# Kernel tuning notes

Measured on AMD Instinct MI355X. Metric: run time of the kernel, lower is better.

## Reference

```python
import jax, jax.numpy as jnp
import numpy as np

B, N, H, W_SP, DIM, FPN = 16, 4, 32, 32, 1024, 512
EPS = 1e-5

def setup_inputs() -> dict:
    key = jax.random.key(0)
    k1, k2 = jax.random.split(key)
    x = jax.random.normal(k1, (B, N, H, W_SP, DIM), dtype=jnp.float32)
    gamma = jnp.ones((DIM,), dtype=jnp.float32)
    beta = jnp.zeros((DIM,), dtype=jnp.float32)
    W = jax.random.normal(k2, (4 * FPN, DIM), dtype=jnp.float32) * (1.0 / np.sqrt(DIM))
    b = jnp.zeros((4 * FPN,), dtype=jnp.float32)
    return {"x": x, "gamma": gamma, "beta": beta, "W": W, "b": b}

def reference(x, gamma, beta, W, b):
    # LayerNorm over channel dim
    mu = jnp.mean(x, axis=-1, keepdims=True)
    var = jnp.mean(jnp.square(x - mu), axis=-1, keepdims=True)
    xn = (x - mu) * jax.lax.rsqrt(var + EPS) * gamma + beta
    # Linear: dim -> 4*fpn_dim (QLinear with quant=False == nn.Linear)
    y = jnp.einsum('bnhwc,oc->bnhwo', xn, W) + b
    # QAct with quant=False is identity.
    # Patch split: (B,N,H,W,2,2,F) -> (B,N,H,2,W,2,F) -> (B,N,2H,2W,F)
    Bv, Nv, Hv, Wv = y.shape[:4]
    y = y.reshape(Bv, Nv, Hv, Wv, 2, 2, FPN)
    y = jnp.transpose(y, (0, 1, 2, 4, 3, 5, 6))
    return y.reshape(Bv, Nv, 2 * Hv, 2 * Wv, FPN)
```

## Files before the change

kernel.cpp:

```cpp
#include <hip/hip_runtime.h>
#include <hip/hip_bf16.h>
#include <cstdint>
#include <cstddef>

#define M_ROWS 65536
#define K_DIM  1024
#define N_OUT  2048

typedef __attribute__((ext_vector_type(8))) short short8;
typedef __attribute__((ext_vector_type(4))) float floatx4;

__device__ __forceinline__ unsigned short f2bf(float f) {
  unsigned int u = __float_as_uint(f);
  u += 0x7fffu + ((u >> 16) & 1u);
  return (unsigned short)(u >> 16);
}

__global__ __launch_bounds__(256) void ln_bf16_kernel(
    const float* __restrict__ x, const float* __restrict__ gamma,
    const float* __restrict__ beta, ushort* __restrict__ xn) {
  const int wave = threadIdx.x >> 6;
  const int lane = threadIdx.x & 63;
  const size_t row = (size_t)blockIdx.x * 4 + wave;
  const float4* xr = (const float4*)(x + row * K_DIM);
  float4 v[4];
  float s = 0.f, ss = 0.f;
#pragma unroll
  for (int i = 0; i < 4; ++i) {
    v[i] = xr[lane + 64 * i];
    s  += v[i].x + v[i].y + v[i].z + v[i].w;
    ss += v[i].x * v[i].x + v[i].y * v[i].y + v[i].z * v[i].z + v[i].w * v[i].w;
  }
#pragma unroll
  for (int off = 32; off; off >>= 1) {
    s  += __shfl_xor(s, off, 64);
    ss += __shfl_xor(ss, off, 64);
  }
  const float mu = s * (1.0f / 1024.0f);
  const float rstd = rsqrtf(ss * (1.0f / 1024.0f) - mu * mu + 1e-5f);
  ushort4* orow = (ushort4*)(xn + row * K_DIM);
#pragma unroll
  for (int i = 0; i < 4; ++i) {
    const float4 g  = ((const float4*)gamma)[lane + 64 * i];
    const float4 bb = ((const float4*)beta)[lane + 64 * i];
    ushort4 o;
    o.x = f2bf((v[i].x - mu) * rstd * g.x + bb.x);
    o.y = f2bf((v[i].y - mu) * rstd * g.y + bb.y);
    o.z = f2bf((v[i].z - mu) * rstd * g.z + bb.z);
    o.w = f2bf((v[i].w - mu) * rstd * g.w + bb.w);
    orow[lane + 64 * i] = o;
  }
}

__global__ __launch_bounds__(256) void wconv_kernel(const float* __restrict__ W,
                                                    ushort* __restrict__ Wb) {
  const int i = blockIdx.x * 256 + threadIdx.x;
  const float4 w = ((const float4*)W)[i];
  ushort4 o;
  o.x = f2bf(w.x); o.y = f2bf(w.y); o.z = f2bf(w.z); o.w = f2bf(w.w);
  ((ushort4*)Wb)[i] = o;
}

__device__ __forceinline__ void async_copy16(const ushort* g, ushort* l) {
  __builtin_amdgcn_global_load_lds(
      (const __attribute__((address_space(1))) void*)g,
      (__attribute__((address_space(3))) void*)l, 16, 0, 0);
}

__global__ __launch_bounds__(256) void gemm_kernel(
    const ushort* __restrict__ A,
    const ushort* __restrict__ Bw,
    const float* __restrict__ bias, float* __restrict__ out) {
  __shared__ ushort As[128 * 32];
  __shared__ ushort Bs[128 * 32];

  const int tid  = threadIdx.x;
  const int bn   = blockIdx.x;
  const int bm   = blockIdx.y;
  const int lane = tid & 63;
  const int warp = tid >> 6;
  const int quad = lane >> 4;
  const int l16  = lane & 15;
  const int wm   = warp & 1;
  const int wn   = warp >> 1;

  const ushort* aG0 = A  + (size_t)(bm * 128      + (tid >> 2)) * K_DIM + (tid & 3) * 8;
  const ushort* aG1 = A  + (size_t)(bm * 128 + 64 + (tid >> 2)) * K_DIM + (tid & 3) * 8;
  const ushort* bG0 = Bw + (size_t)(bn * 128      + (tid >> 2)) * K_DIM + (tid & 3) * 8;
  const ushort* bG1 = Bw + (size_t)(bn * 128 + 64 + (tid >> 2)) * K_DIM + (tid & 3) * 8;
  ushort* lA0 = As + tid * 8;
  ushort* lA1 = As + 2048 + tid * 8;
  ushort* lB0 = Bs + tid * 8;
  ushort* lB1 = Bs + 2048 + tid * 8;

  const ushort* as_base = As + (wm * 64 + l16) * 32 + quad * 8;
  const ushort* bs_base = Bs + (wn * 64 + l16) * 32 + quad * 8;

  floatx4 acc[4][4] = {};

  for (int kt = 0; kt < K_DIM / 32; ++kt) {
    const int k0 = kt * 32;
    async_copy16(aG0 + k0, lA0);
    async_copy16(aG1 + k0, lA1);
    async_copy16(bG0 + k0, lB0);
    async_copy16(bG1 + k0, lB1);
    __syncthreads();

    short8 af[4], bf[4];
#pragma unroll
    for (int i = 0; i < 4; ++i) af[i] = *(const short8*)(as_base + i * 16 * 32);
#pragma unroll
    for (int i = 0; i < 4; ++i) bf[i] = *(const short8*)(bs_base + i * 16 * 32);
#pragma unroll
    for (int mi = 0; mi < 4; ++mi)
#pragma unroll
      for (int ni = 0; ni < 4; ++ni)
        acc[mi][ni] = __builtin_amdgcn_mfma_f32_16x16x32_bf16(
            af[mi], bf[ni], acc[mi][ni], 0, 0, 0);
    __syncthreads();
  }

  float bv[4];
#pragma unroll
  for (int ni = 0; ni < 4; ++ni)
    bv[ni] = bias[bn * 128 + wn * 64 + ni * 16 + l16];

#pragma unroll
  for (int mi = 0; mi < 4; ++mi) {
    const int mrow = bm * 128 + wm * 64 + mi * 16 + quad * 4;
#pragma unroll
    for (int r = 0; r < 4; ++r) {
      const int m = mrow + r;
      const int bnn = m >> 10;
      const int h = (m >> 5) & 31;
      const int w = m & 31;
      const size_t rowbase = (((size_t)(bnn * 64 + 2 * h)) * 64 + 2 * w) * 512;
#pragma unroll
      for (int ni = 0; ni < 4; ++ni) {
        const int o = bn * 128 + wn * 64 + ni * 16 + l16;
        const int p1 = (o >> 10) & 1;
        const int p2 = (o >> 9) & 1;
        const int f = o & 511;
        out[rowbase + (size_t)p1 * 32768 + (size_t)p2 * 512 + f] =
            acc[mi][ni][r] + bv[ni];
      }
    }
  }
}

__global__ __launch_bounds__(256) void fused_fallback(
    const float* __restrict__ x, const float* __restrict__ gamma,
    const float* __restrict__ beta, const float* __restrict__ W,
    const float* __restrict__ b, float* __restrict__ out) {
  __shared__ float xs[1024];
  __shared__ float red[8];
  const int m = blockIdx.x;
  const int t = threadIdx.x;
  const float4 v = ((const float4*)(x + (size_t)m * 1024))[t];
  float s = v.x + v.y + v.z + v.w;
  float ss = v.x * v.x + v.y * v.y + v.z * v.z + v.w * v.w;
#pragma unroll
  for (int off = 32; off; off >>= 1) {
    s  += __shfl_xor(s, off, 64);
    ss += __shfl_xor(ss, off, 64);
  }
  if ((t & 63) == 0) { red[t >> 6] = s; red[4 + (t >> 6)] = ss; }
  __syncthreads();
  const float S = red[0] + red[1] + red[2] + red[3];
  const float SS = red[4] + red[5] + red[6] + red[7];
  const float mu = S * (1.0f / 1024.0f);
  const float rstd = rsqrtf(SS * (1.0f / 1024.0f) - mu * mu + 1e-5f);
  const float4 g = ((const float4*)gamma)[t];
  const float4 be = ((const float4*)beta)[t];
  float4 xn;
  xn.x = (v.x - mu) * rstd * g.x + be.x;
  xn.y = (v.y - mu) * rstd * g.y + be.y;
  xn.z = (v.z - mu) * rstd * g.z + be.z;
  xn.w = (v.w - mu) * rstd * g.w + be.w;
  ((float4*)xs)[t] = xn;
  __syncthreads();
  const int bnn = m >> 10, h = (m >> 5) & 31, w = m & 31;
  const size_t rowbase = (((size_t)(bnn * 64 + 2 * h)) * 64 + 2 * w) * 512;
#pragma unroll 1
  for (int i = 0; i < 8; ++i) {
    const int o = t + i * 256;
    const float4* wr = (const float4*)(W + (size_t)o * 1024);
    float acc = 0.f;
    for (int k = 0; k < 256; ++k) {
      const float4 wv = wr[k];
      const float4 xv = ((const float4*)xs)[k];
      acc += wv.x * xv.x + wv.y * xv.y + wv.z * xv.z + wv.w * xv.w;
    }
    const int p1 = (o >> 10) & 1, p2 = (o >> 9) & 1, f = o & 511;
    out[rowbase + (size_t)p1 * 32768 + (size_t)p2 * 512 + f] = acc + b[o];
  }
}

extern "C" void kernel_launch(void* const* d_in, const int* in_sizes, int n_in,
                              void* d_out, int out_size, void* d_ws, size_t ws_size,
                              hipStream_t stream) {
  const float* x     = (const float*)d_in[0];
  const float* gamma = (const float*)d_in[1];
  const float* beta  = (const float*)d_in[2];
  const float* W     = (const float*)d_in[3];
  const float* b     = (const float*)d_in[4];
  float* out = (float*)d_out;

  const size_t xn_bytes = (size_t)M_ROWS * K_DIM * 2;
  const size_t wb_bytes = (size_t)N_OUT * K_DIM * 2;
  if (ws_size >= xn_bytes + wb_bytes) {
    ushort* xn = (ushort*)d_ws;
    ushort* Wb = (ushort*)((char*)d_ws + xn_bytes);
    ln_bf16_kernel<<<M_ROWS / 4, 256, 0, stream>>>(x, gamma, beta, xn);
    wconv_kernel<<<(N_OUT * K_DIM / 4) / 256, 256, 0, stream>>>(W, Wb);
    gemm_kernel<<<dim3(N_OUT / 128, M_ROWS / 128), 256, 0, stream>>>(xn, Wb, b, out);
  } else {
    fused_fallback<<<M_ROWS, 256, 0, stream>>>(x, gamma, beta, W, b, out);
  }
}
```

Before: 1.017 ms.

## Rewrite GEMM with 256x256 tiles, double-buffered swizzled LDS, and XCD-aware block remap

Replaces the 128x128 single-buffered GEMM with a 256x256 tile, 512-thread kernel using BK=64 and two LDS buffers. Global-to-LDS async copies for the next tiles are interleaved with MFMA work in quarter steps, with explicit waitcnt and barrier control plus XOR swizzling to avoid LDS bank conflicts. Block IDs are remapped so consecutive blocks spread across XCDs and share B tiles. The aim is to hide memory latency and raise MFMA utilisation. The cost is 128KB of LDS per block and fragile hand-placed synchronisation.

```diff
diff --git a/kernel.cpp b/kernel.cpp
--- a/kernel.cpp
+++ b/kernel.cpp
@@ -6,6 +6,7 @@
 #define M_ROWS 65536
 #define K_DIM  1024
 #define N_OUT  2048
+#define NTILE  16
 
 typedef __attribute__((ext_vector_type(8))) short short8;
 typedef __attribute__((ext_vector_type(4))) float floatx4;
@@ -67,77 +68,131 @@
       (__attribute__((address_space(3))) void*)l, 16, 0, 0);
 }
 
-__global__ __launch_bounds__(256) void gemm_kernel(
+__global__ __launch_bounds__(512, 2) void gemm_kernel(
     const ushort* __restrict__ A,
     const ushort* __restrict__ Bw,
     const float* __restrict__ bias, float* __restrict__ out) {
-  __shared__ ushort As[128 * 32];
-  __shared__ ushort Bs[128 * 32];
-
-  const int tid  = threadIdx.x;
-  const int bn   = blockIdx.x;
-  const int bm   = blockIdx.y;
+  __shared__ ushort As[2][256 * 64];
+  __shared__ ushort Bs[2][256 * 64];
+
+  const int tid = threadIdx.x;
+  const int bid = blockIdx.x;
+  const int wg  = (bid & 7) * 256 + (bid >> 3);
+  const int bn  = wg & 7;
+  const int bm  = wg >> 3;
+
   const int lane = tid & 63;
-  const int warp = tid >> 6;
+  const int wv   = tid >> 6;
+  const int wm   = wv & 1;
+  const int wn   = wv >> 1;
   const int quad = lane >> 4;
   const int l16  = lane & 15;
-  const int wm   = warp & 1;
-  const int wn   = warp >> 1;
-
-  const ushort* aG0 = A  + (size_t)(bm * 128      + (tid >> 2)) * K_DIM + (tid & 3) * 8;
-  const ushort* aG1 = A  + (size_t)(bm * 128 + 64 + (tid >> 2)) * K_DIM + (tid & 3) * 8;
-  const ushort* bG0 = Bw + (size_t)(bn * 128      + (tid >> 2)) * K_DIM + (tid & 3) * 8;
-  const ushort* bG1 = Bw + (size_t)(bn * 128 + 64 + (tid >> 2)) * K_DIM + (tid & 3) * 8;
-  ushort* lA0 = As + tid * 8;
-  ushort* lA1 = As + 2048 + tid * 8;
-  ushort* lB0 = Bs + tid * 8;
-  ushort* lB1 = Bs + 2048 + tid * 8;
-
-  const ushort* as_base = As + (wm * 64 + l16) * 32 + quad * 8;
-  const ushort* bs_base = Bs + (wn * 64 + l16) * 32 + quad * 8;
-
-  floatx4 acc[4][4] = {};
-
-  for (int kt = 0; kt < K_DIM / 32; ++kt) {
-    const int k0 = kt * 32;
-    async_copy16(aG0 + k0, lA0);
-    async_copy16(aG1 + k0, lA1);
-    async_copy16(bG0 + k0, lB0);
-    async_copy16(bG1 + k0, lB1);
-    __syncthreads();
-
-    short8 af[4], bf[4];
-#pragma unroll
-    for (int i = 0; i < 4; ++i) af[i] = *(const short8*)(as_base + i * 16 * 32);
-#pragma unroll
-    for (int i = 0; i < 4; ++i) bf[i] = *(const short8*)(bs_base + i * 16 * 32);
-#pragma unroll
-    for (int mi = 0; mi < 4; ++mi)
-#pragma unroll
-      for (int ni = 0; ni < 4; ++ni)
-        acc[mi][ni] = __builtin_amdgcn_mfma_f32_16x16x32_bf16(
-            af[mi], bf[ni], acc[mi][ni], 0, 0, 0);
-    __syncthreads();
-  }
-
+  const int swz  = (l16 & 7) << 4;
+
+  const int srow = tid >> 3;
+  const int scol = ((tid & 7) ^ (srow & 7)) * 8;
+  const ushort* Ag = A  + (size_t)(bm * 256 + srow) * K_DIM + scol;
+  const ushort* Bg = Bw + (size_t)(bn * 256 + srow) * K_DIM + scol;
+  ushort* Ad = &As[0][0] + srow * 64 + (tid & 7) * 8;
+  ushort* Bd = &Bs[0][0] + srow * 64 + (tid & 7) * 8;
+
+#define STAGE_A(buf, h, kt) do {                                         \
+    const ushort* g_ = Ag + (size_t)((h) * 128) * K_DIM + (kt) * 64;     \
+    ushort* l_ = Ad + (buf) * 16384 + (h) * 8192;                        \
+    async_copy16(g_, l_);                                                \
+    async_copy16(g_ + (size_t)64 * K_DIM, l_ + 4096);                    \
+  } while (0)
+#define STAGE_B(buf, h, kt) do {                                         \
+    const ushort* g_ = Bg + (size_t)((h) * 128) * K_DIM + (kt) * 64;     \
+    ushort* l_ = Bd + (buf) * 16384 + (h) * 8192;                        \
+    async_copy16(g_, l_);                                                \
+    async_copy16(g_ + (size_t)64 * K_DIM, l_ + 4096);                    \
+  } while (0)
+
+  STAGE_A(0, 0, 0); STAGE_A(0, 1, 0);
+  STAGE_B(0, 0, 0); STAGE_B(0, 1, 0);
+  STAGE_B(1, 0, 1); STAGE_B(1, 1, 1);
+  asm volatile("s_waitcnt vmcnt(4)" ::: "memory");
+  __builtin_amdgcn_s_barrier();
+  asm volatile("" ::: "memory");
+
+  floatx4 acc[8][4] = {};
+  const char* AsB = (const char*)&As[0][0];
+  const char* BsB = (const char*)&Bs[0][0];
+
+#pragma unroll 1
+  for (int t = 0; t < NTILE; ++t) {
+    const char* Ab = AsB + (t & 1) * 32768;
+    const char* Bb = BsB + (t & 1) * 32768;
+    short8 bfr[4][2];
+#pragma unroll
+    for (int q = 0; q < 4; ++q) {
+      short8 afr[2][2];
+      if (q == 0) {
+#pragma unroll
+        for (int ni = 0; ni < 4; ++ni)
+#pragma unroll
+          for (int ks = 0; ks < 2; ++ks)
+            bfr[ni][ks] = *(const short8*)(
+                Bb + (wn * 64 + ni * 16 + l16) * 128 +
+                ((ks * 64 + quad * 16) ^ swz));
+      }
+#pragma unroll
+      for (int j = 0; j < 2; ++j)
+#pragma unroll
+        for (int ks = 0; ks < 2; ++ks)
+          afr[j][ks] = *(const short8*)(
+              Ab + (wm * 128 + (q * 2 + j) * 16 + l16) * 128 +
+              ((ks * 64 + quad * 16) ^ swz));
+
+      if (q == 0)      { if (t + 1 < NTILE) STAGE_A((t + 1) & 1, 0, t + 1); }
+      else if (q == 1) { if (t + 1 < NTILE) STAGE_A((t + 1) & 1, 1, t + 1); }
+      else if (q == 2) { if (t + 2 < NTILE) STAGE_B(t & 1, 0, t + 2); }
+      else             { if (t + 2 < NTILE) STAGE_B(t & 1, 1, t + 2); }
+
+      __builtin_amdgcn_s_barrier();
+      asm volatile("s_waitcnt lgkmcnt(0)" ::: "memory");
+      __builtin_amdgcn_sched_barrier(0);
+      __builtin_amdgcn_s_setprio(1);
+#pragma unroll
+      for (int j = 0; j < 2; ++j)
+#pragma unroll
+        for (int ni = 0; ni < 4; ++ni)
+#pragma unroll
+          for (int ks = 0; ks < 2; ++ks)
+            acc[q * 2 + j][ni] = __builtin_amdgcn_mfma_f32_16x16x32_bf16(
+                afr[j][ks], bfr[ni][ks], acc[q * 2 + j][ni], 0, 0, 0);
+      __builtin_amdgcn_s_setprio(0);
+
+      if (q == 3) {
+        if (t == NTILE - 2)     asm volatile("s_waitcnt vmcnt(0)" ::: "memory");
+        else if (t < NTILE - 2) asm volatile("s_waitcnt vmcnt(4)" ::: "memory");
+      }
+      __builtin_amdgcn_s_barrier();
+      asm volatile("" ::: "memory");
+    }
+  }
+#undef STAGE_A
+#undef STAGE_B
+
+  const int obase = bn * 256 + wn * 64;
   float bv[4];
 #pragma unroll
-  for (int ni = 0; ni < 4; ++ni)
-    bv[ni] = bias[bn * 128 + wn * 64 + ni * 16 + l16];
-
-#pragma unroll
-  for (int mi = 0; mi < 4; ++mi) {
-    const int mrow = bm * 128 + wm * 64 + mi * 16 + quad * 4;
+  for (int ni = 0; ni < 4; ++ni) bv[ni] = bias[obase + ni * 16 + l16];
+
+#pragma unroll
+  for (int mi = 0; mi < 8; ++mi) {
+    const int m0 = bm * 256 + wm * 128 + mi * 16 + quad * 4;
 #pragma unroll
     for (int r = 0; r < 4; ++r) {
-      const int m = mrow + r;
+      const int m = m0 + r;
       const int bnn = m >> 10;
       const int h = (m >> 5) & 31;
       const int w = m & 31;
       const size_t rowbase = (((size_t)(bnn * 64 + 2 * h)) * 64 + 2 * w) * 512;
 #pragma unroll
       for (int ni = 0; ni < 4; ++ni) {
-        const int o = bn * 128 + wn * 64 + ni * 16 + l16;
+        const int o = obase + ni * 16 + l16;
         const int p1 = (o >> 10) & 1;
         const int p2 = (o >> 9) & 1;
         const int f = o & 511;
@@ -213,7 +268,7 @@
     ushort* Wb = (ushort*)((char*)d_ws + xn_bytes);
     ln_bf16_kernel<<<M_ROWS / 4, 256, 0, stream>>>(x, gamma, beta, xn);
     wconv_kernel<<<(N_OUT * K_DIM / 4) / 256, 256, 0, stream>>>(W, Wb);
-    gemm_kernel<<<dim3(N_OUT / 128, M_ROWS / 128), 256, 0, stream>>>(xn, Wb, b, out);
+    gemm_kernel<<<(M_ROWS / 256) * (N_OUT / 256), 512, 0, stream>>>(xn, Wb, b, out);
   } else {
     fused_fallback<<<M_ROWS, 256, 0, stream>>>(x, gamma, beta, W, b, out);
   }
```

Result: no change. 1.006 ms (-1.1%).
